# Kernel optimization log

Measured on AMD Instinct MI355X. Metric: run time of the kernel, lower is better.

The kernel has to match this reference:

```python
import jax, jax.numpy as jnp
import numpy as np

B, T, D_IN, D_OUT = 64, 1024, 512, 512


def setup_inputs() -> dict:
    key = jax.random.key(0)
    k_x, k_w, k_wr = jax.random.split(key, 3)
    x = jax.random.normal(k_x, (B, T, D_IN), dtype=jnp.float32)
    # glorot_uniform for W
    limit = np.sqrt(6.0 / (D_IN + D_OUT)).astype(np.float32)
    W = jax.random.uniform(k_w, (D_IN, D_OUT), dtype=jnp.float32, minval=-limit, maxval=limit)
    # orthogonal for W_recurrent
    a = jax.random.normal(k_wr, (D_OUT, D_OUT), dtype=jnp.float32)
    q, r = jnp.linalg.qr(a)
    W_recurrent = q * jnp.sign(jnp.diag(r))[None, :]
    b = jnp.zeros((D_OUT,), dtype=jnp.float32)
    return {"x": x, "W": W, "W_recurrent": W_recurrent, "b": b}


def reference(x, W, W_recurrent, b):
    # x: [B, T, D_in]; sequential tanh RNN; return last hidden state [B, D_out]
    x_t = jnp.transpose(x, (1, 0, 2))  # [T, B, D_in]
    h0 = jnp.zeros((x.shape[0], W.shape[1]), dtype=x.dtype)

    def step(h, xt):
        h_new = jnp.tanh(xt @ W + h @ W_recurrent + b)
        return h_new, None

    h_last, _ = jax.lax.scan(step, h0, x_t)
    return h_last
```

## Files before the change

kernel.cpp:

```cpp
#include <hip/hip_runtime.h>
#include <math.h>

#define BATCH   64
#define TSTEPS  1024
#define DIN     512
#define DH      512
#define MDIM    (BATCH * TSTEPS)

#define MB          16
#define HSTRIDE_W   260
#define H_WORDS     (16 * HSTRIDE_W)
#define SLICE_WORDS (16 * HSTRIDE_W)
#define WRL_WORDS   (8 * SLICE_WORDS)
#define K2_LDS_WORDS (WRL_WORDS + H_WORDS)
#define K2_LDS_BYTES (K2_LDS_WORDS * 4)

typedef _Float16 f16x8 __attribute__((ext_vector_type(8)));
typedef float    f32x4 __attribute__((ext_vector_type(4)));

__device__ inline unsigned short f2h_bits(float x) {
    _Float16 h = (_Float16)x;
    return __builtin_bit_cast(unsigned short, h);
}
__device__ inline float ftanh(float x) {
    float e = __builtin_amdgcn_exp2f(x * 2.88539008177792681472f);
    return 1.0f - 2.0f * __builtin_amdgcn_rcpf(e + 1.0f);
}

__global__ __launch_bounds__(256) void convert_x(const float* __restrict__ x,
                                                 _Float16* __restrict__ xh,
                                                 int nvec) {
    int i = blockIdx.x * blockDim.x + threadIdx.x;
    int stride = gridDim.x * blockDim.x;
    for (; i < nvec; i += stride) {
        const float4* p = (const float4*)x + 2 * (size_t)i;
        float4 a = p[0], b = p[1];
        f16x8 o = { (_Float16)a.x, (_Float16)a.y, (_Float16)a.z, (_Float16)a.w,
                    (_Float16)b.x, (_Float16)b.y, (_Float16)b.z, (_Float16)b.w };
        ((f16x8*)xh)[i] = o;
    }
}

__global__ __launch_bounds__(256) void transpose_w(const float* __restrict__ W,
                                                   _Float16* __restrict__ Wt) {
    __shared__ float tile[64][65];
    const int t  = threadIdx.x;
    const int c  = t & 63;
    const int r0 = t >> 6;
    const int bn = blockIdx.x & 7;
    const int bk = blockIdx.x >> 3;
    const int k0 = bk * 64, n0 = bn * 64;
    #pragma unroll
    for (int i = 0; i < 16; ++i)
        tile[r0 + 4 * i][c] = W[(size_t)(k0 + r0 + 4 * i) * DH + n0 + c];
    __syncthreads();
    #pragma unroll
    for (int i = 0; i < 16; ++i)
        Wt[(size_t)(n0 + r0 + 4 * i) * DIN + k0 + c] = (_Float16)tile[c][r0 + 4 * i];
}

__global__ __launch_bounds__(256) void gemm_xw_mfma(const _Float16* __restrict__ Xh,
                                                    const _Float16* __restrict__ Wt,
                                                    const float* __restrict__ bias,
                                                    float* __restrict__ XW) {
    __shared__ __align__(16) _Float16 Ah[128][32];
    __shared__ __align__(16) _Float16 Bh[128][32];

    const int tid  = threadIdx.x;
    const int wv   = tid >> 6;
    const int lane = tid & 63;
    const int bn   = blockIdx.x & 3;
    const int bm   = blockIdx.x >> 2;
    const int m0   = bm * 128;
    const int n0   = bn * 128;

    const int mbase = (wv >> 1) * 64;
    const int nbase = (wv & 1) * 64;
    const int fr    = lane & 15;
    const int fq    = lane >> 4;

    f32x4 acc[4][4];
    #pragma unroll
    for (int i = 0; i < 4; ++i)
        #pragma unroll
        for (int j = 0; j < 4; ++j)
            acc[i][j] = (f32x4){0.f, 0.f, 0.f, 0.f};

    for (int kc = 0; kc < DIN / 32; ++kc) {
        const int k0 = kc * 32;
#if __has_builtin(__builtin_amdgcn_global_load_lds)
        #pragma unroll
        for (int q = 0; q < 2; ++q) {
            const int rb = wv * 2 + q;
            const int gr = (rb * 16) + (lane >> 2);
            const int gc = (lane & 3) * 8;
            const _Float16* ga = Xh + (size_t)(m0 + gr) * DIN + k0 + gc;
            const _Float16* gb = Wt + (size_t)(n0 + gr) * DIN + k0 + gc;
            __builtin_amdgcn_global_load_lds(
                (const __attribute__((address_space(1))) void*)ga,
                (__attribute__((address_space(3))) void*)&Ah[rb * 16][0], 16, 0, 0);
            __builtin_amdgcn_global_load_lds(
                (const __attribute__((address_space(1))) void*)gb,
                (__attribute__((address_space(3))) void*)&Bh[rb * 16][0], 16, 0, 0);
        }
#else
        #pragma unroll
        for (int q = 0; q < 2; ++q) {
            const int h0 = (q * 256 + tid) * 8;
            const int row = h0 >> 5, col = h0 & 31;
            *((uint4*)Ah + (q * 256 + tid)) =
                *(const uint4*)(Xh + (size_t)(m0 + row) * DIN + k0 + col);
            *((uint4*)Bh + (q * 256 + tid)) =
                *(const uint4*)(Wt + (size_t)(n0 + row) * DIN + k0 + col);
        }
#endif
        __syncthreads();

        f16x8 af[4], bf[4];
        #pragma unroll
        for (int mt = 0; mt < 4; ++mt)
            af[mt] = *(const f16x8*)&Ah[mbase + mt * 16 + fr][fq * 8];
        #pragma unroll
        for (int nt = 0; nt < 4; ++nt)
            bf[nt] = *(const f16x8*)&Bh[nbase + nt * 16 + fr][fq * 8];
        #pragma unroll
        for (int mt = 0; mt < 4; ++mt)
            #pragma unroll
            for (int nt = 0; nt < 4; ++nt)
                acc[mt][nt] = __builtin_amdgcn_mfma_f32_16x16x32_f16(
                    af[mt], bf[nt], acc[mt][nt], 0, 0, 0);
        __syncthreads();
    }

    #pragma unroll
    for (int nt = 0; nt < 4; ++nt) {
        const int col = n0 + nbase + nt * 16 + fr;
        const float bvl = bias[col];
        #pragma unroll
        for (int mt = 0; mt < 4; ++mt) {
            #pragma unroll
            for (int r = 0; r < 4; ++r) {
                const int row = m0 + mbase + mt * 16 + fq * 4 + r;
                XW[(size_t)row * DH + col] = acc[mt][nt][r] + bvl;
            }
        }
    }
}

__global__ __launch_bounds__(256) void gemm_xw(const float* __restrict__ X,
                                               const float* __restrict__ W,
                                               const float* __restrict__ bias,
                                               float* __restrict__ XW) {
    __shared__ float As[16][68];
    __shared__ float Bs[16][68];
    const int tid = threadIdx.x;
    const int bx  = blockIdx.x & 7;
    const int by  = blockIdx.x >> 3;
    const int m0  = by * 64, n0 = bx * 64;
    const int ty = tid >> 4, tx = tid & 15;
    const int arow = tid >> 2, akq = (tid & 3) * 4;
    const int brow = tid >> 4, bcq = (tid & 15) * 4;
    float acc[4][4] = {{0.f}};
    for (int k0 = 0; k0 < DIN; k0 += 16) {
        float4 av = *(const float4*)&X[(size_t)(m0 + arow) * DIN + k0 + akq];
        float4 bv = *(const float4*)&W[(size_t)(k0 + brow) * DH + n0 + bcq];
        __syncthreads();
        As[akq + 0][arow] = av.x; As[akq + 1][arow] = av.y;
        As[akq + 2][arow] = av.z; As[akq + 3][arow] = av.w;
        *(float4*)&Bs[brow][bcq] = bv;
        __syncthreads();
        #pragma unroll
        for (int k = 0; k < 16; ++k) {
            float4 a = *(const float4*)&As[k][ty * 4];
            float4 b = *(const float4*)&Bs[k][tx * 4];
            float ar[4] = {a.x, a.y, a.z, a.w};
            float br[4] = {b.x, b.y, b.z, b.w};
            #pragma unroll
            for (int i = 0; i < 4; ++i)
                #pragma unroll
                for (int j = 0; j < 4; ++j)
                    acc[i][j] = fmaf(ar[i], br[j], acc[i][j]);
        }
    }
    float4 bv = *(const float4*)&bias[n0 + tx * 4];
    const float br[4] = {bv.x, bv.y, bv.z, bv.w};
    #pragma unroll
    for (int i = 0; i < 4; ++i) {
        float4 o;
        o.x = acc[i][0] + br[0]; o.y = acc[i][1] + br[1];
        o.z = acc[i][2] + br[2]; o.w = acc[i][3] + br[3];
        *(float4*)&XW[(size_t)(m0 + ty * 4 + i) * DH + n0 + tx * 4] = o;
    }
}

__global__ __launch_bounds__(512, 2) void rnn_scan4(const float* __restrict__ XW,
                                                    const float* __restrict__ Wr,
                                                    float* __restrict__ Hout) {
    extern __shared__ unsigned int lds[];
    unsigned int*   wrl = lds;
    unsigned int*   hb  = lds + WRL_WORDS;
    unsigned short* hsh = (unsigned short*)hb;

    const int tid  = threadIdx.x;
    const int wv   = tid >> 6;
    const int lane = tid & 63;
    const int fr   = lane & 15;
    const int fq   = lane >> 4;
    const int b0   = blockIdx.x * MB;

    for (int i = tid; i < H_WORDS; i += 512) hb[i] = 0u;

    f16x8 breg[3][16];
    #pragma unroll
    for (int s = 0; s < 3; ++s) {
        const int col = wv * 64 + s * 16 + fr;
        #pragma unroll
        for (int c = 0; c < 16; ++c) {
            const int k0 = c * 32 + fq * 8;
            f16x8 v;
            #pragma unroll
            for (int j = 0; j < 8; ++j)
                v[j] = (_Float16)Wr[(size_t)(k0 + j) * DH + col];
            breg[s][c] = v;
        }
    }
    {
        const int col = wv * 64 + 48 + fr;
        unsigned int* base = wrl + wv * SLICE_WORDS + fr * HSTRIDE_W + fq * 4;
        #pragma unroll
        for (int c = 0; c < 16; ++c) {
            const int k0 = c * 32 + fq * 8;
            f16x8 v;
            #pragma unroll
            for (int j = 0; j < 8; ++j)
                v[j] = (_Float16)Wr[(size_t)(k0 + j) * DH + col];
            *(uint4*)(base + c * 16) = __builtin_bit_cast(uint4, v);
        }
    }
    __syncthreads();

    const float* xwt = XW + (size_t)(b0 + fq * 4) * TSTEPS * DH + wv * 64 + fr;
    const unsigned int* abase = hb + fr * HSTRIDE_W + fq * 4;
    const unsigned int* bbase = wrl + wv * SLICE_WORDS + fr * HSTRIDE_W + fq * 4;

    #pragma unroll 1
    for (int t = 0; t < TSTEPS; ++t) {
        f32x4 cc[4];
        #pragma unroll
        for (int s = 0; s < 4; ++s) cc[s] = (f32x4){0.f, 0.f, 0.f, 0.f};

        #pragma unroll
        for (int c = 0; c < 16; ++c) {
            f16x8 af = __builtin_bit_cast(f16x8, *(const uint4*)(abase + c * 16));
            f16x8 bf = __builtin_bit_cast(f16x8, *(const uint4*)(bbase + c * 16));
            cc[0] = __builtin_amdgcn_mfma_f32_16x16x32_f16(af, breg[0][c], cc[0], 0, 0, 0);
            cc[1] = __builtin_amdgcn_mfma_f32_16x16x32_f16(af, breg[1][c], cc[1], 0, 0, 0);
            cc[2] = __builtin_amdgcn_mfma_f32_16x16x32_f16(af, breg[2][c], cc[2], 0, 0, 0);
            cc[3] = __builtin_amdgcn_mfma_f32_16x16x32_f16(af, bf,         cc[3], 0, 0, 0);
        }

        float xv[4][4];
        #pragma unroll
        for (int s = 0; s < 4; ++s)
            #pragma unroll
            for (int r = 0; r < 4; ++r)
                xv[s][r] = xwt[(size_t)r * TSTEPS * DH + (size_t)t * DH + s * 16];

        __syncthreads();

        #pragma unroll
        for (int s = 0; s < 4; ++s) {
            #pragma unroll
            for (int r = 0; r < 4; ++r) {
                float h = ftanh(cc[s][r] + xv[s][r]);
                hsh[(fq * 4 + r) * (HSTRIDE_W * 2) + wv * 64 + s * 16 + fr] = f2h_bits(h);
            }
        }
        __syncthreads();
    }

    {
        const int m  = tid >> 5;
        const int cb = (tid & 31) * 16;
        #pragma unroll
        for (int g = 0; g < 16; g += 8) {
            f16x8 v = __builtin_bit_cast(f16x8,
                *(const uint4*)(hsh + (size_t)m * (HSTRIDE_W * 2) + cb + g));
            float4 o0 = { (float)v[0], (float)v[1], (float)v[2], (float)v[3] };
            float4 o1 = { (float)v[4], (float)v[5], (float)v[6], (float)v[7] };
            *(float4*)&Hout[(size_t)(b0 + m) * DH + cb + g]     = o0;
            *(float4*)&Hout[(size_t)(b0 + m) * DH + cb + g + 4] = o1;
        }
    }
}

extern "C" void kernel_launch(void* const* d_in, const int* in_sizes, int n_in,
                              void* d_out, int out_size, void* d_ws, size_t ws_size,
                              hipStream_t stream) {
    const float* x  = (const float*)d_in[0];
    const float* W  = (const float*)d_in[1];
    const float* Wr = (const float*)d_in[2];
    const float* bv = (const float*)d_in[3];
    float* out = (float*)d_out;

    const size_t XW_BYTES = (size_t)MDIM * DH * sizeof(float);
    const size_t XH_BYTES = (size_t)MDIM * DIN * sizeof(_Float16);
    const size_t WT_BYTES = (size_t)DIN * DH * sizeof(_Float16);
    if (ws_size < XW_BYTES) return;

    float* xw = (float*)d_ws;

    hipFuncSetAttribute((const void*)rnn_scan4,
                        hipFuncAttributeMaxDynamicSharedMemorySize, K2_LDS_BYTES);

    if (ws_size >= XW_BYTES + XH_BYTES + WT_BYTES) {
        _Float16* xh = (_Float16*)((char*)d_ws + XW_BYTES);
        _Float16* wt = (_Float16*)((char*)d_ws + XW_BYTES + XH_BYTES);
        convert_x<<<dim3(2048), dim3(256), 0, stream>>>(x, xh, MDIM * DIN / 8);
        transpose_w<<<dim3(64), dim3(256), 0, stream>>>(W, wt);
        gemm_xw_mfma<<<dim3((MDIM / 128) * (DH / 128)), dim3(256), 0, stream>>>(
            xh, wt, bv, xw);
    } else {
        gemm_xw<<<dim3((MDIM / 64) * (DH / 64)), dim3(256), 0, stream>>>(x, W, bv, xw);
    }

    rnn_scan4<<<dim3(BATCH / MB), dim3(512), K2_LDS_BYTES, stream>>>(xw, Wr, out);
}
```

Before: 2.080 ms.

## Split recurrent scan across paired blocks exchanging hidden halves via global flags

The recurrent scan now runs on 8 workgroups instead of 4. Each pair of workgroups owns one 16-row batch group and splits the 512 output columns between them. Every step, each block publishes its half of the new hidden state to a double-buffered global array and signals the peer with a release flag. The peer spin-waits on that flag before reading the data, and overlaps the MFMAs on its own half with the wait. This halves each block's per-step MFMA work and lets all of W_recurrent live in registers, which removes the LDS weight slice, at the cost of a cross-CU handshake on every timestep. The spin loop gives up after a bounded count, which could silently produce wrong results if the peer falls behind.

New measurement: 2.450 ms. 17.8% more time.

```diff
diff --git a/kernel.cpp b/kernel.cpp
--- a/kernel.cpp
+++ b/kernel.cpp
@@ -6,14 +6,7 @@
 #define DIN     512
 #define DH      512
 #define MDIM    (BATCH * TSTEPS)
-
-#define MB          16
-#define HSTRIDE_W   260
-#define H_WORDS     (16 * HSTRIDE_W)
-#define SLICE_WORDS (16 * HSTRIDE_W)
-#define WRL_WORDS   (8 * SLICE_WORDS)
-#define K2_LDS_WORDS (WRL_WORDS + H_WORDS)
-#define K2_LDS_BYTES (K2_LDS_WORDS * 4)
+#define MB      16
 
 typedef _Float16 f16x8 __attribute__((ext_vector_type(8)));
 typedef float    f32x4 __attribute__((ext_vector_type(4)));
@@ -193,104 +186,131 @@
     }
 }
 
-__global__ __launch_bounds__(512, 2) void rnn_scan4(const float* __restrict__ XW,
-                                                    const float* __restrict__ Wr,
-                                                    float* __restrict__ Hout) {
-    extern __shared__ unsigned int lds[];
-    unsigned int*   wrl = lds;
-    unsigned int*   hb  = lds + WRL_WORDS;
-    unsigned short* hsh = (unsigned short*)hb;
+__global__ __launch_bounds__(512, 2) void rnn_scan8(const float* __restrict__ XW,
+                                                    const _Float16* __restrict__ Wrt,
+                                                    float* __restrict__ Hout,
+                                                    unsigned short* __restrict__ hbuf,
+                                                    unsigned int* __restrict__ flags) {
+    __shared__ __align__(16) _Float16 H[8192];
 
     const int tid  = threadIdx.x;
+    const int bid  = blockIdx.x;
+    const int g    = bid >> 1;
+    const int p    = bid & 1;
+    const int peer = bid ^ 1;
     const int wv   = tid >> 6;
     const int lane = tid & 63;
     const int fr   = lane & 15;
     const int fq   = lane >> 4;
-    const int b0   = blockIdx.x * MB;
-
-    for (int i = tid; i < H_WORDS; i += 512) hb[i] = 0u;
-
-    f16x8 breg[3][16];
-    #pragma unroll
-    for (int s = 0; s < 3; ++s) {
-        const int col = wv * 64 + s * 16 + fr;
-        #pragma unroll
-        for (int c = 0; c < 16; ++c) {
-            const int k0 = c * 32 + fq * 8;
-            f16x8 v;
-            #pragma unroll
-            for (int j = 0; j < 8; ++j)
-                v[j] = (_Float16)Wr[(size_t)(k0 + j) * DH + col];
-            breg[s][c] = v;
-        }
-    }
-    {
-        const int col = wv * 64 + 48 + fr;
-        unsigned int* base = wrl + wv * SLICE_WORDS + fr * HSTRIDE_W + fq * 4;
-        #pragma unroll
-        for (int c = 0; c < 16; ++c) {
-            const int k0 = c * 32 + fq * 8;
-            f16x8 v;
-            #pragma unroll
-            for (int j = 0; j < 8; ++j)
-                v[j] = (_Float16)Wr[(size_t)(k0 + j) * DH + col];
-            *(uint4*)(base + c * 16) = __builtin_bit_cast(uint4, v);
+    const int b0   = g * MB;
+    const int colbase = p * 256 + wv * 32;
+
+    for (int i = tid; i < 4096; i += 512) ((unsigned int*)H)[i] = 0u;
+
+    f16x8 breg[2][16];
+    #pragma unroll
+    for (int s = 0; s < 2; ++s) {
+        const int col = colbase + s * 16 + fr;
+        #pragma unroll
+        for (int i = 0; i < 16; ++i) {
+            const int cabs = (i < 8) ? (8 * p + i) : (8 * (1 - p) + (i - 8));
+            breg[s][i] = *(const f16x8*)&Wrt[(size_t)col * DIN + cabs * 32 + fq * 8];
         }
     }
     __syncthreads();
 
-    const float* xwt = XW + (size_t)(b0 + fq * 4) * TSTEPS * DH + wv * 64 + fr;
-    const unsigned int* abase = hb + fr * HSTRIDE_W + fq * 4;
-    const unsigned int* bbase = wrl + wv * SLICE_WORDS + fr * HSTRIDE_W + fq * 4;
+    unsigned short* myhb0   = hbuf + (size_t)bid  * 8192;
+    unsigned short* peerhb0 = hbuf + (size_t)peer * 8192;
+    unsigned int*   myflag   = flags + bid  * 64;
+    unsigned int*   peerflag = flags + peer * 64;
+
+    const int ownB  = p * 8192;
+    const int peerB = 8192 - ownB;
+    char* Hb = (char*)H;
+
+    const float* xbase = XW + (size_t)(b0 + fq * 4) * TSTEPS * DH + colbase + fr;
+
+    const int epi_slotbase = (fr >> 3) * 16 + fq * 4;
+    const int epi_off = (8 * p + wv) * 512 + (fr & 7);
+    const int ghb_off = wv * 512 + (fr & 7);
 
     #pragma unroll 1
     for (int t = 0; t < TSTEPS; ++t) {
-        f32x4 cc[4];
-        #pragma unroll
-        for (int s = 0; s < 4; ++s) cc[s] = (f32x4){0.f, 0.f, 0.f, 0.f};
-
-        #pragma unroll
-        for (int c = 0; c < 16; ++c) {
-            f16x8 af = __builtin_bit_cast(f16x8, *(const uint4*)(abase + c * 16));
-            f16x8 bf = __builtin_bit_cast(f16x8, *(const uint4*)(bbase + c * 16));
-            cc[0] = __builtin_amdgcn_mfma_f32_16x16x32_f16(af, breg[0][c], cc[0], 0, 0, 0);
-            cc[1] = __builtin_amdgcn_mfma_f32_16x16x32_f16(af, breg[1][c], cc[1], 0, 0, 0);
-            cc[2] = __builtin_amdgcn_mfma_f32_16x16x32_f16(af, breg[2][c], cc[2], 0, 0, 0);
-            cc[3] = __builtin_amdgcn_mfma_f32_16x16x32_f16(af, bf,         cc[3], 0, 0, 0);
-        }
-
-        float xv[4][4];
-        #pragma unroll
-        for (int s = 0; s < 4; ++s)
+        unsigned long long pl0 = 0, pl1 = 0;
+        if (t > 0) {
+            if (tid == 0) {
+                unsigned spins = 0;
+                while (__hip_atomic_load(peerflag, __ATOMIC_ACQUIRE,
+                                         __HIP_MEMORY_SCOPE_AGENT) < (unsigned)t) {
+                    if (++spins > (1u << 17)) break;
+                }
+            }
+            __syncthreads();
+            unsigned long long* src =
+                (unsigned long long*)(peerhb0 + (size_t)(t & 1) * 4096) + tid * 2;
+            pl0 = __hip_atomic_load(src,     __ATOMIC_RELAXED, __HIP_MEMORY_SCOPE_AGENT);
+            pl1 = __hip_atomic_load(src + 1, __ATOMIC_RELAXED, __HIP_MEMORY_SCOPE_AGENT);
+        }
+
+        f32x4 cc0 = {0.f, 0.f, 0.f, 0.f}, cc1 = {0.f, 0.f, 0.f, 0.f};
+
+        #pragma unroll
+        for (int i = 0; i < 8; ++i) {
+            f16x8 af = *(const f16x8*)(Hb + ownB + i * 1024 + lane * 16);
+            cc0 = __builtin_amdgcn_mfma_f32_16x16x32_f16(af, breg[0][i], cc0, 0, 0, 0);
+            cc1 = __builtin_amdgcn_mfma_f32_16x16x32_f16(af, breg[1][i], cc1, 0, 0, 0);
+        }
+
+        float xv[2][4];
+        #pragma unroll
+        for (int s = 0; s < 2; ++s)
             #pragma unroll
             for (int r = 0; r < 4; ++r)
-                xv[s][r] = xwt[(size_t)r * TSTEPS * DH + (size_t)t * DH + s * 16];
-
-        __syncthreads();
-
-        #pragma unroll
-        for (int s = 0; s < 4; ++s) {
+                xv[s][r] = xbase[(size_t)r * TSTEPS * DH + (size_t)t * DH + s * 16];
+
+        if (t > 0) {
+            unsigned long long* dst = (unsigned long long*)(Hb + peerB + tid * 16);
+            dst[0] = pl0; dst[1] = pl1;
+        }
+        __syncthreads();
+
+        #pragma unroll
+        for (int i = 8; i < 16; ++i) {
+            f16x8 af = *(const f16x8*)(Hb + peerB + (i - 8) * 1024 + lane * 16);
+            cc0 = __builtin_amdgcn_mfma_f32_16x16x32_f16(af, breg[0][i], cc0, 0, 0, 0);
+            cc1 = __builtin_amdgcn_mfma_f32_16x16x32_f16(af, breg[1][i], cc1, 0, 0, 0);
+        }
+
+        unsigned short* myhb = myhb0 + (size_t)((t + 1) & 1) * 4096;
+        #pragma unroll
+        for (int s = 0; s < 2; ++s) {
             #pragma unroll
             for (int r = 0; r < 4; ++r) {
-                float h = ftanh(cc[s][r] + xv[s][r]);
-                hsh[(fq * 4 + r) * (HSTRIDE_W * 2) + wv * 64 + s * 16 + fr] = f2h_bits(h);
+                const float a = (s == 0 ? cc0[r] : cc1[r]) + xv[s][r];
+                const unsigned short hb16 = f2h_bits(ftanh(a));
+                const int slot = epi_slotbase + s * 32 + r;
+                ((unsigned short*)H)[epi_off + slot * 8] = hb16;
+                __hip_atomic_store(myhb + ghb_off + slot * 8, hb16,
+                                   __ATOMIC_RELAXED, __HIP_MEMORY_SCOPE_AGENT);
             }
         }
         __syncthreads();
+        if (tid == 0)
+            __hip_atomic_store(myflag, (unsigned)(t + 1),
+                               __ATOMIC_RELEASE, __HIP_MEMORY_SCOPE_AGENT);
     }
 
     {
-        const int m  = tid >> 5;
-        const int cb = (tid & 31) * 16;
-        #pragma unroll
-        for (int g = 0; g < 16; g += 8) {
-            f16x8 v = __builtin_bit_cast(f16x8,
-                *(const uint4*)(hsh + (size_t)m * (HSTRIDE_W * 2) + cb + g));
-            float4 o0 = { (float)v[0], (float)v[1], (float)v[2], (float)v[3] };
-            float4 o1 = { (float)v[4], (float)v[5], (float)v[6], (float)v[7] };
-            *(float4*)&Hout[(size_t)(b0 + m) * DH + cb + g]     = o0;
-            *(float4*)&Hout[(size_t)(b0 + m) * DH + cb + g + 4] = o1;
-        }
+        const int m    = tid >> 5;
+        const int cg   = tid & 31;
+        const int cabs = 8 * p + (cg >> 2);
+        const int fqp  = cg & 3;
+        f16x8 v = *(const f16x8*)(Hb + cabs * 1024 + (fqp * 16 + m) * 16);
+        const int col = p * 256 + cg * 8;
+        float4 o0 = { (float)v[0], (float)v[1], (float)v[2], (float)v[3] };
+        float4 o1 = { (float)v[4], (float)v[5], (float)v[6], (float)v[7] };
+        *(float4*)&Hout[(size_t)(b0 + m) * DH + col]     = o0;
+        *(float4*)&Hout[(size_t)(b0 + m) * DH + col + 4] = o1;
     }
 }
 
@@ -303,19 +323,28 @@
     const float* bv = (const float*)d_in[3];
     float* out = (float*)d_out;
 
-    const size_t XW_BYTES = (size_t)MDIM * DH * sizeof(float);
-    const size_t XH_BYTES = (size_t)MDIM * DIN * sizeof(_Float16);
-    const size_t WT_BYTES = (size_t)DIN * DH * sizeof(_Float16);
-    if (ws_size < XW_BYTES) return;
-
-    float* xw = (float*)d_ws;
-
-    hipFuncSetAttribute((const void*)rnn_scan4,
-                        hipFuncAttributeMaxDynamicSharedMemorySize, K2_LDS_BYTES);
-
-    if (ws_size >= XW_BYTES + XH_BYTES + WT_BYTES) {
-        _Float16* xh = (_Float16*)((char*)d_ws + XW_BYTES);
-        _Float16* wt = (_Float16*)((char*)d_ws + XW_BYTES + XH_BYTES);
+    const size_t XW_BYTES   = (size_t)MDIM * DH * sizeof(float);
+    const size_t HBUF_BYTES = (size_t)8 * 2 * 4096 * sizeof(unsigned short);
+    const size_t FLAG_BYTES = (size_t)8 * 64 * sizeof(unsigned int);
+    const size_t WRT_BYTES  = (size_t)DH * DH * sizeof(_Float16);
+    const size_t XH_BYTES   = (size_t)MDIM * DIN * sizeof(_Float16);
+    const size_t WT_BYTES   = (size_t)DIN * DH * sizeof(_Float16);
+
+    const size_t SCAN_MIN = XW_BYTES + HBUF_BYTES + FLAG_BYTES + WRT_BYTES;
+    if (ws_size < SCAN_MIN) return;
+
+    char* base = (char*)d_ws;
+    float*          xw    = (float*)base;
+    unsigned short* hbuf  = (unsigned short*)(base + XW_BYTES);
+    unsigned int*   flags = (unsigned int*)(base + XW_BYTES + HBUF_BYTES);
+    _Float16*       wrt   = (_Float16*)(base + XW_BYTES + HBUF_BYTES + FLAG_BYTES);
+
+    hipMemsetAsync(flags, 0, FLAG_BYTES, stream);
+    transpose_w<<<dim3(64), dim3(256), 0, stream>>>(Wr, wrt);
+
+    if (ws_size >= SCAN_MIN + XH_BYTES + WT_BYTES) {
+        _Float16* xh = (_Float16*)(base + SCAN_MIN);
+        _Float16* wt = (_Float16*)(base + SCAN_MIN + XH_BYTES);
         convert_x<<<dim3(2048), dim3(256), 0, stream>>>(x, xh, MDIM * DIN / 8);
         transpose_w<<<dim3(64), dim3(256), 0, stream>>>(W, wt);
         gemm_xw_mfma<<<dim3((MDIM / 128) * (DH / 128)), dim3(256), 0, stream>>>(
@@ -324,5 +353,5 @@
         gemm_xw<<<dim3((MDIM / 64) * (DH / 64)), dim3(256), 0, stream>>>(x, W, bv, xw);
     }
 
-    rnn_scan4<<<dim3(BATCH / MB), dim3(512), K2_LDS_BYTES, stream>>>(xw, Wr, out);
-}
+    rnn_scan8<<<dim3(8), dim3(512), 0, stream>>>(xw, wrt, out, hbuf, flags);
+}
```

## Keep full recurrent weight slice in registers and double-buffer hidden state

Applied to the files above, without the earlier changes.

The scan kernel now holds all four 16-column slices of the recurrent weight in registers instead of spilling one slice to LDS. It loads them as vectors from a pre-transposed fp16 copy made by an extra transpose kernel. The hidden state is double-buffered in a small static LDS array laid out in MFMA fragment order, which removes one barrier per timestep and makes the A-operand reads contiguous. The XW loads are also issued before the MFMA chain. The cost is higher register pressure, which may cause spills or limit occupancy, plus an extra transpose launch.

Result: slower. 5.612 ms (+169.8%).

```diff
diff --git a/kernel.cpp b/kernel.cpp
--- a/kernel.cpp
+++ b/kernel.cpp
@@ -6,14 +6,7 @@
 #define DIN     512
 #define DH      512
 #define MDIM    (BATCH * TSTEPS)
-
-#define MB          16
-#define HSTRIDE_W   260
-#define H_WORDS     (16 * HSTRIDE_W)
-#define SLICE_WORDS (16 * HSTRIDE_W)
-#define WRL_WORDS   (8 * SLICE_WORDS)
-#define K2_LDS_WORDS (WRL_WORDS + H_WORDS)
-#define K2_LDS_BYTES (K2_LDS_WORDS * 4)
+#define MB      16
 
 typedef _Float16 f16x8 __attribute__((ext_vector_type(8)));
 typedef float    f32x4 __attribute__((ext_vector_type(4)));
@@ -193,13 +186,10 @@
     }
 }
 
-__global__ __launch_bounds__(512, 2) void rnn_scan4(const float* __restrict__ XW,
-                                                    const float* __restrict__ Wr,
-                                                    float* __restrict__ Hout) {
-    extern __shared__ unsigned int lds[];
-    unsigned int*   wrl = lds;
-    unsigned int*   hb  = lds + WRL_WORDS;
-    unsigned short* hsh = (unsigned short*)hb;
+__global__ __launch_bounds__(512, 2) void rnn_scan_res(const float* __restrict__ XW,
+                                                       const _Float16* __restrict__ Wrt,
+                                                       float* __restrict__ Hout) {
+    __shared__ __align__(16) _Float16 H[2][8192];
 
     const int tid  = threadIdx.x;
     const int wv   = tid >> 6;
@@ -208,72 +198,54 @@
     const int fq   = lane >> 4;
     const int b0   = blockIdx.x * MB;
 
-    for (int i = tid; i < H_WORDS; i += 512) hb[i] = 0u;
-
-    f16x8 breg[3][16];
-    #pragma unroll
-    for (int s = 0; s < 3; ++s) {
+    for (int i = tid; i < 4096; i += 512) ((unsigned int*)H[0])[i] = 0u;
+
+    f16x8 breg[4][16];
+    #pragma unroll
+    for (int s = 0; s < 4; ++s) {
         const int col = wv * 64 + s * 16 + fr;
         #pragma unroll
-        for (int c = 0; c < 16; ++c) {
-            const int k0 = c * 32 + fq * 8;
-            f16x8 v;
-            #pragma unroll
-            for (int j = 0; j < 8; ++j)
-                v[j] = (_Float16)Wr[(size_t)(k0 + j) * DH + col];
-            breg[s][c] = v;
-        }
-    }
-    {
-        const int col = wv * 64 + 48 + fr;
-        unsigned int* base = wrl + wv * SLICE_WORDS + fr * HSTRIDE_W + fq * 4;
-        #pragma unroll
-        for (int c = 0; c < 16; ++c) {
-            const int k0 = c * 32 + fq * 8;
-            f16x8 v;
-            #pragma unroll
-            for (int j = 0; j < 8; ++j)
-                v[j] = (_Float16)Wr[(size_t)(k0 + j) * DH + col];
-            *(uint4*)(base + c * 16) = __builtin_bit_cast(uint4, v);
-        }
+        for (int c = 0; c < 16; ++c)
+            breg[s][c] = *(const f16x8*)&Wrt[(size_t)col * DH + c * 32 + fq * 8];
     }
     __syncthreads();
 
-    const float* xwt = XW + (size_t)(b0 + fq * 4) * TSTEPS * DH + wv * 64 + fr;
-    const unsigned int* abase = hb + fr * HSTRIDE_W + fq * 4;
-    const unsigned int* bbase = wrl + wv * SLICE_WORDS + fr * HSTRIDE_W + fq * 4;
+    const float* xbase = XW + (size_t)(b0 + fq * 4) * TSTEPS * DH + wv * 64 + fr;
+
+    const int ebase = wv * 1024 + ((fr >> 3) * 16 + fq * 4) * 8 + (fr & 7);
 
     #pragma unroll 1
     for (int t = 0; t < TSTEPS; ++t) {
+        const _Float16* Hr = H[t & 1];
+        _Float16*       Hw = H[(t + 1) & 1];
+
+        float xv[4][4];
+        #pragma unroll
+        for (int s = 0; s < 4; ++s)
+            #pragma unroll
+            for (int r = 0; r < 4; ++r)
+                xv[s][r] = xbase[(size_t)r * TSTEPS * DH + (size_t)t * DH + s * 16];
+
         f32x4 cc[4];
         #pragma unroll
         for (int s = 0; s < 4; ++s) cc[s] = (f32x4){0.f, 0.f, 0.f, 0.f};
 
         #pragma unroll
         for (int c = 0; c < 16; ++c) {
-            f16x8 af = __builtin_bit_cast(f16x8, *(const uint4*)(abase + c * 16));
-            f16x8 bf = __builtin_bit_cast(f16x8, *(const uint4*)(bbase + c * 16));
+            f16x8 af = *(const f16x8*)((const char*)Hr + c * 1024 + lane * 16);
             cc[0] = __builtin_amdgcn_mfma_f32_16x16x32_f16(af, breg[0][c], cc[0], 0, 0, 0);
             cc[1] = __builtin_amdgcn_mfma_f32_16x16x32_f16(af, breg[1][c], cc[1], 0, 0, 0);
             cc[2] = __builtin_amdgcn_mfma_f32_16x16x32_f16(af, breg[2][c], cc[2], 0, 0, 0);
-            cc[3] = __builtin_amdgcn_mfma_f32_16x16x32_f16(af, bf,         cc[3], 0, 0, 0);
-        }
-
-        float xv[4][4];
-        #pragma unroll
-        for (int s = 0; s < 4; ++s)
-            #pragma unroll
-            for (int r = 0; r < 4; ++r)
-                xv[s][r] = xwt[(size_t)r * TSTEPS * DH + (size_t)t * DH + s * 16];
-
-        __syncthreads();
+            cc[3] = __builtin_amdgcn_mfma_f32_16x16x32_f16(af, breg[3][c], cc[3], 0, 0, 0);
+        }
 
         #pragma unroll
         for (int s = 0; s < 4; ++s) {
             #pragma unroll
             for (int r = 0; r < 4; ++r) {
-                float h = ftanh(cc[s][r] + xv[s][r]);
-                hsh[(fq * 4 + r) * (HSTRIDE_W * 2) + wv * 64 + s * 16 + fr] = f2h_bits(h);
+                const float a = cc[s][r] + xv[s][r];
+                ((unsigned short*)Hw)[ebase + (s >> 1) * 512 + (s & 1) * 256 + r * 8] =
+                    f2h_bits(ftanh(a));
             }
         }
         __syncthreads();
@@ -281,15 +253,18 @@
 
     {
         const int m  = tid >> 5;
-        const int cb = (tid & 31) * 16;
-        #pragma unroll
-        for (int g = 0; g < 16; g += 8) {
-            f16x8 v = __builtin_bit_cast(f16x8,
-                *(const uint4*)(hsh + (size_t)m * (HSTRIDE_W * 2) + cb + g));
+        const int cg = tid & 31;
+        const int cb = cg * 16;
+        const int c  = cg >> 1;
+        const int fb = (cg & 1) * 2;
+        const char* Hb = (const char*)H[0];
+        #pragma unroll
+        for (int g = 0; g < 2; ++g) {
+            f16x8 v = *(const f16x8*)(Hb + c * 1024 + ((fb + g) * 16 + m) * 16);
             float4 o0 = { (float)v[0], (float)v[1], (float)v[2], (float)v[3] };
             float4 o1 = { (float)v[4], (float)v[5], (float)v[6], (float)v[7] };
-            *(float4*)&Hout[(size_t)(b0 + m) * DH + cb + g]     = o0;
-            *(float4*)&Hout[(size_t)(b0 + m) * DH + cb + g + 4] = o1;
+            *(float4*)&Hout[(size_t)(b0 + m) * DH + cb + g * 8]     = o0;
+            *(float4*)&Hout[(size_t)(b0 + m) * DH + cb + g * 8 + 4] = o1;
         }
     }
 }
@@ -303,19 +278,23 @@
     const float* bv = (const float*)d_in[3];
     float* out = (float*)d_out;
 
-    const size_t XW_BYTES = (size_t)MDIM * DH * sizeof(float);
-    const size_t XH_BYTES = (size_t)MDIM * DIN * sizeof(_Float16);
-    const size_t WT_BYTES = (size_t)DIN * DH * sizeof(_Float16);
-    if (ws_size < XW_BYTES) return;
-
-    float* xw = (float*)d_ws;
-
-    hipFuncSetAttribute((const void*)rnn_scan4,
-                        hipFuncAttributeMaxDynamicSharedMemorySize, K2_LDS_BYTES);
-
-    if (ws_size >= XW_BYTES + XH_BYTES + WT_BYTES) {
-        _Float16* xh = (_Float16*)((char*)d_ws + XW_BYTES);
-        _Float16* wt = (_Float16*)((char*)d_ws + XW_BYTES + XH_BYTES);
+    const size_t XW_BYTES  = (size_t)MDIM * DH * sizeof(float);
+    const size_t WRT_BYTES = (size_t)DH * DH * sizeof(_Float16);
+    const size_t XH_BYTES  = (size_t)MDIM * DIN * sizeof(_Float16);
+    const size_t WT_BYTES  = (size_t)DIN * DH * sizeof(_Float16);
+
+    const size_t SCAN_MIN = XW_BYTES + WRT_BYTES;
+    if (ws_size < SCAN_MIN) return;
+
+    char* base = (char*)d_ws;
+    float*    xw  = (float*)base;
+    _Float16* wrt = (_Float16*)(base + XW_BYTES);
+
+    transpose_w<<<dim3(64), dim3(256), 0, stream>>>(Wr, wrt);
+
+    if (ws_size >= SCAN_MIN + XH_BYTES + WT_BYTES) {
+        _Float16* xh = (_Float16*)(base + SCAN_MIN);
+        _Float16* wt = (_Float16*)(base + SCAN_MIN + XH_BYTES);
         convert_x<<<dim3(2048), dim3(256), 0, stream>>>(x, xh, MDIM * DIN / 8);
         transpose_w<<<dim3(64), dim3(256), 0, stream>>>(W, wt);
         gemm_xw_mfma<<<dim3((MDIM / 128) * (DH / 128)), dim3(256), 0, stream>>>(
@@ -324,5 +303,5 @@
         gemm_xw<<<dim3((MDIM / 64) * (DH / 64)), dim3(256), 0, stream>>>(x, W, bv, xw);
     }
 
-    rnn_scan4<<<dim3(BATCH / MB), dim3(512), K2_LDS_BYTES, stream>>>(xw, Wr, out);
-}
+    rnn_scan_res<<<dim3(BATCH / MB), dim3(512), 0, stream>>>(xw, wrt, out);
+}
```
